# Kernel tuning notes

Measured on AMD Instinct MI355X. Metric: run time of the kernel, lower is better.

Reference implementation:

```python
import jax, jax.numpy as jnp
import numpy as np

MARGIN = 40.0


def setup_inputs() -> dict:
    key = jax.random.key(0)
    k1, k2 = jax.random.split(key)
    feat = jax.random.normal(k1, (4096, 512), dtype=jnp.float32)
    targets = jax.random.randint(k2, (4096,), 0, 64, dtype=jnp.int64)
    return {"feat": feat, "targets": targets}


def reference(feat, targets):
    # corr: (n, n) Gram matrix of features
    corr = feat @ feat.T
    # mask[i, j] = True if same class
    mask = targets[:, None] == targets[None, :]
    big = jnp.asarray(jnp.finfo(corr.dtype).max, corr.dtype)
    # per-row min over positives, max over negatives
    corr_ap = jnp.min(jnp.where(mask, corr, big), axis=1)
    corr_an = jnp.max(jnp.where(mask, -big, corr), axis=1)
    # MarginRankingLoss(margin=40) with y = 1: mean(relu(-(ap - an) + margin))
    loss = jnp.mean(jax.nn.relu(corr_an - corr_ap + MARGIN))
    return loss
```

## Files before the change

### kernel.cpp

```cpp
#include <hip/hip_runtime.h>
#include <float.h>
#include <stdint.h>


#define N_ROWS 4096
#define D_K    512
#define BM     128
#define BN     128
#define BK     32
#define NJT    (N_ROWS / BN)
#define MARGIN 40.0f

typedef __bf16 bf16_t;
typedef bf16_t bf16x8 __attribute__((ext_vector_type(8)));
typedef float  floatx4 __attribute__((ext_vector_type(4)));
typedef unsigned short ushort_t;

#define GLOAD_LDS16(g, l)                                        \
    __builtin_amdgcn_global_load_lds(                            \
        (const __attribute__((address_space(1))) void*)(g),      \
        (__attribute__((address_space(3))) void*)(l), 16, 0, 0)

__device__ __forceinline__ ushort_t f2bf_rne(float x) {
    uint32_t u = __builtin_bit_cast(uint32_t, x);
    return (ushort_t)((u + 0x7FFFu + ((u >> 16) & 1u)) >> 16);
}

typedef ushort_t ushortx8 __attribute__((ext_vector_type(8)));

__global__ __launch_bounds__(256) void cast_kernel(
    const float* __restrict__ f, ushort_t* __restrict__ o)
{
    const int i = (blockIdx.x * 256 + threadIdx.x) * 8;
    const float4 v0 = *(const float4*)(f + i);
    const float4 v1 = *(const float4*)(f + i + 4);
    ushortx8 r;
    r[0] = f2bf_rne(v0.x); r[1] = f2bf_rne(v0.y);
    r[2] = f2bf_rne(v0.z); r[3] = f2bf_rne(v0.w);
    r[4] = f2bf_rne(v1.x); r[5] = f2bf_rne(v1.y);
    r[6] = f2bf_rne(v1.z); r[7] = f2bf_rne(v1.w);
    *(ushortx8*)(o + i) = r;
}

__global__ __launch_bounds__(256) void gram_mfma_kernel(
    const ushort_t* __restrict__ fb, const int* __restrict__ tgt,
    float* __restrict__ ap_part, float* __restrict__ an_part)
{
    __shared__ __align__(16) ushort_t As[BM * BK];
    __shared__ __align__(16) ushort_t Bs[BN * BK];
    __shared__ int tgI[BM];
    __shared__ int tgJ[BN];
    __shared__ float apRed[2][BM];
    __shared__ float anRed[2][BM];

    const int tid  = threadIdx.x;
    const int i0   = blockIdx.y * BM;
    const int j0   = blockIdx.x * BN;
    const int lane = tid & 63;
    const int wave = tid >> 6;
    const int wr   = wave >> 1;
    const int wc   = wave & 1;
    const int lr   = lane & 15;
    const int lg   = lane >> 4;

    if (tid < BM)            tgI[tid]       = tgt[i0 + tid];
    else if (tid < BM + BN)  tgJ[tid - BM]  = tgt[j0 + tid - BM];

    const int srow = tid >> 2;
    const int skq  = tid & 3;
    const size_t gA0 = (size_t)(i0 + srow) * D_K + skq * 8;
    const size_t gB0 = (size_t)(j0 + srow) * D_K + skq * 8;
    char* AsB = (char*)As;
    char* BsB = (char*)Bs;

    floatx4 acc[4][4];
#pragma unroll
    for (int a = 0; a < 4; ++a)
#pragma unroll
        for (int b = 0; b < 4; ++b) acc[a][b] = (floatx4)0.0f;

    for (int k0 = 0; k0 < D_K; k0 += BK) {
        GLOAD_LDS16(fb + gA0 + k0,               AsB + tid * 16);
        GLOAD_LDS16(fb + gA0 + k0 + 64 * D_K,    AsB + 4096 + tid * 16);
        GLOAD_LDS16(fb + gB0 + k0,               BsB + tid * 16);
        GLOAD_LDS16(fb + gB0 + k0 + 64 * D_K,    BsB + 4096 + tid * 16);
        __syncthreads();

        bf16x8 af[4], bf[4];
#pragma unroll
        for (int rg = 0; rg < 4; ++rg)
            af[rg] = *(const bf16x8*)(As + ((wr * 64 + rg * 16 + lr) * BK + lg * 8));
#pragma unroll
        for (int cg = 0; cg < 4; ++cg)
            bf[cg] = *(const bf16x8*)(Bs + ((wc * 64 + cg * 16 + lr) * BK + lg * 8));
#pragma unroll
        for (int rg = 0; rg < 4; ++rg)
#pragma unroll
            for (int cg = 0; cg < 4; ++cg)
                acc[rg][cg] = __builtin_amdgcn_mfma_f32_16x16x32_bf16(
                    af[rg], bf[cg], acc[rg][cg], 0, 0, 0);
        __syncthreads();
    }

    int tj[4];
#pragma unroll
    for (int cg = 0; cg < 4; ++cg) tj[cg] = tgJ[wc * 64 + cg * 16 + lr];

#pragma unroll
    for (int rg = 0; rg < 4; ++rg) {
#pragma unroll
        for (int r = 0; r < 4; ++r) {
            const int rloc = wr * 64 + rg * 16 + lg * 4 + r;
            const int ti = tgI[rloc];
            float vap = FLT_MAX, van = -FLT_MAX;
#pragma unroll
            for (int cg = 0; cg < 4; ++cg) {
                const float v = acc[rg][cg][r];
                if (ti == tj[cg]) vap = fminf(vap, v);
                else              van = fmaxf(van, v);
            }
#pragma unroll
            for (int m = 1; m < 16; m <<= 1) {
                vap = fminf(vap, __shfl_xor(vap, m));
                van = fmaxf(van, __shfl_xor(van, m));
            }
            if (lr == 0) { apRed[wc][rloc] = vap; anRed[wc][rloc] = van; }
        }
    }
    __syncthreads();

    if (tid < BM) {
        ap_part[(size_t)blockIdx.x * N_ROWS + i0 + tid] =
            fminf(apRed[0][tid], apRed[1][tid]);
        an_part[(size_t)blockIdx.x * N_ROWS + i0 + tid] =
            fmaxf(anRed[0][tid], anRed[1][tid]);
    }
}

__global__ __launch_bounds__(256) void fold_kernel(
    const float* __restrict__ ap_part, const float* __restrict__ an_part,
    float* __restrict__ out)
{
    __shared__ float sred[4];
    const int tid = threadIdx.x;
    const int row = blockIdx.x * 256 + tid;
    float ap = FLT_MAX, an = -FLT_MAX;
#pragma unroll
    for (int js = 0; js < NJT; ++js) {
        ap = fminf(ap, ap_part[(size_t)js * N_ROWS + row]);
        an = fmaxf(an, an_part[(size_t)js * N_ROWS + row]);
    }
    const float v = an - ap + MARGIN;
    float s = (v > 0.0f) ? v : 0.0f;
#pragma unroll
    for (int m = 32; m >= 1; m >>= 1) s += __shfl_down(s, m);
    if ((tid & 63) == 0) sred[tid >> 6] = s;
    __syncthreads();
    if (tid == 0)
        atomicAdd(out, (sred[0] + sred[1] + sred[2] + sred[3]) * (1.0f / N_ROWS));
}

extern "C" void kernel_launch(void* const* d_in, const int* in_sizes, int n_in,
                              void* d_out, int out_size, void* d_ws, size_t ws_size,
                              hipStream_t stream)
{
    const float* feat = (const float*)d_in[0];
    const int*   tgt  = (const int*)d_in[1];

    ushort_t* fb      = (ushort_t*)d_ws;
    float*    ap_part = (float*)(fb + (size_t)N_ROWS * D_K);
    float*    an_part = ap_part + (size_t)NJT * N_ROWS;

    cast_kernel<<<(N_ROWS * D_K) / (256 * 8), 256, 0, stream>>>(feat, fb);

    dim3 grid(N_ROWS / BN, N_ROWS / BM);
    gram_mfma_kernel<<<grid, 256, 0, stream>>>(fb, tgt, ap_part, an_part);

    hipMemsetAsync(d_out, 0, sizeof(float), stream);
    fold_kernel<<<N_ROWS / 256, 256, 0, stream>>>(ap_part, an_part, (float*)d_out);
}
```

Baseline: 105.3 us.

## Exploit Gram matrix symmetry by computing only upper-triangular tiles

The Gram kernel now launches only the upper-triangular 128x128 tiles, about half of the original grid. Each off-diagonal tile also produces column-wise min/max reductions, which are written as partials for the transposed rows. The fold kernel becomes a single 1024-thread block that writes the result directly, removing the memset and the atomic. This roughly halves the MFMA work, at the cost of extra epilogue reductions, a small serial tile-index decode loop, and a serialized fold in one block.

```diff
diff --git a/kernel.cpp b/kernel.cpp
--- a/kernel.cpp
+++ b/kernel.cpp
@@ -8,13 +8,15 @@
 #define BM     128
 #define BN     128
 #define BK     32
-#define NJT    (N_ROWS / BN)
+#define NTB    32
+#define NTILES (NTB * (NTB + 1) / 2)
 #define MARGIN 40.0f
 
 typedef __bf16 bf16_t;
 typedef bf16_t bf16x8 __attribute__((ext_vector_type(8)));
 typedef float  floatx4 __attribute__((ext_vector_type(4)));
 typedef unsigned short ushort_t;
+typedef ushort_t ushortx8 __attribute__((ext_vector_type(8)));
 
 #define GLOAD_LDS16(g, l)                                        \
     __builtin_amdgcn_global_load_lds(                            \
@@ -25,8 +27,6 @@
     uint32_t u = __builtin_bit_cast(uint32_t, x);
     return (ushort_t)((u + 0x7FFFu + ((u >> 16) & 1u)) >> 16);
 }
-
-typedef ushort_t ushortx8 __attribute__((ext_vector_type(8)));
 
 __global__ __launch_bounds__(256) void cast_kernel(
     const float* __restrict__ f, ushort_t* __restrict__ o)
@@ -50,12 +50,16 @@
     __shared__ __align__(16) ushort_t Bs[BN * BK];
     __shared__ int tgI[BM];
     __shared__ int tgJ[BN];
-    __shared__ float apRed[2][BM];
-    __shared__ float anRed[2][BM];
+    __shared__ float apRed[2][BM],  anRed[2][BM];
+    __shared__ float apRedT[2][BN], anRedT[2][BN];
+
+    int bi = 0, rem = blockIdx.x;
+    while (rem >= NTB - bi) { rem -= NTB - bi; ++bi; }
+    const int bj = bi + rem;
 
     const int tid  = threadIdx.x;
-    const int i0   = blockIdx.y * BM;
-    const int j0   = blockIdx.x * BN;
+    const int i0   = bi * BM;
+    const int j0   = bj * BN;
     const int lane = tid & 63;
     const int wave = tid >> 6;
     const int wr   = wave >> 1;
@@ -63,8 +67,8 @@
     const int lr   = lane & 15;
     const int lg   = lane >> 4;
 
-    if (tid < BM)            tgI[tid]       = tgt[i0 + tid];
-    else if (tid < BM + BN)  tgJ[tid - BM]  = tgt[j0 + tid - BM];
+    if (tid < BM)            tgI[tid]      = tgt[i0 + tid];
+    else if (tid < BM + BN)  tgJ[tid - BM] = tgt[j0 + tid - BM];
 
     const int srow = tid >> 2;
     const int skq  = tid & 3;
@@ -80,10 +84,10 @@
         for (int b = 0; b < 4; ++b) acc[a][b] = (floatx4)0.0f;
 
     for (int k0 = 0; k0 < D_K; k0 += BK) {
-        GLOAD_LDS16(fb + gA0 + k0,               AsB + tid * 16);
-        GLOAD_LDS16(fb + gA0 + k0 + 64 * D_K,    AsB + 4096 + tid * 16);
-        GLOAD_LDS16(fb + gB0 + k0,               BsB + tid * 16);
-        GLOAD_LDS16(fb + gB0 + k0 + 64 * D_K,    BsB + 4096 + tid * 16);
+        GLOAD_LDS16(fb + gA0 + k0,            AsB + tid * 16);
+        GLOAD_LDS16(fb + gA0 + k0 + 64 * D_K, AsB + 4096 + tid * 16);
+        GLOAD_LDS16(fb + gB0 + k0,            BsB + tid * 16);
+        GLOAD_LDS16(fb + gB0 + k0 + 64 * D_K, BsB + 4096 + tid * 16);
         __syncthreads();
 
         bf16x8 af[4], bf[4];
@@ -106,6 +110,10 @@
 #pragma unroll
     for (int cg = 0; cg < 4; ++cg) tj[cg] = tgJ[wc * 64 + cg * 16 + lr];
 
+    float apT[4], anT[4];
+#pragma unroll
+    for (int cg = 0; cg < 4; ++cg) { apT[cg] = FLT_MAX; anT[cg] = -FLT_MAX; }
+
 #pragma unroll
     for (int rg = 0; rg < 4; ++rg) {
 #pragma unroll
@@ -116,8 +124,8 @@
 #pragma unroll
             for (int cg = 0; cg < 4; ++cg) {
                 const float v = acc[rg][cg][r];
-                if (ti == tj[cg]) vap = fminf(vap, v);
-                else              van = fmaxf(van, v);
+                if (ti == tj[cg]) { vap = fminf(vap, v); apT[cg] = fminf(apT[cg], v); }
+                else              { van = fmaxf(van, v); anT[cg] = fmaxf(anT[cg], v); }
             }
 #pragma unroll
             for (int m = 1; m < 16; m <<= 1) {
@@ -127,37 +135,55 @@
             if (lr == 0) { apRed[wc][rloc] = vap; anRed[wc][rloc] = van; }
         }
     }
+#pragma unroll
+    for (int cg = 0; cg < 4; ++cg) {
+        float vap = apT[cg], van = anT[cg];
+        vap = fminf(vap, __shfl_xor(vap, 16)); van = fmaxf(van, __shfl_xor(van, 16));
+        vap = fminf(vap, __shfl_xor(vap, 32)); van = fmaxf(van, __shfl_xor(van, 32));
+        if (lg == 0) {
+            apRedT[wr][wc * 64 + cg * 16 + lr] = vap;
+            anRedT[wr][wc * 64 + cg * 16 + lr] = van;
+        }
+    }
     __syncthreads();
 
     if (tid < BM) {
-        ap_part[(size_t)blockIdx.x * N_ROWS + i0 + tid] =
-            fminf(apRed[0][tid], apRed[1][tid]);
-        an_part[(size_t)blockIdx.x * N_ROWS + i0 + tid] =
-            fmaxf(anRed[0][tid], anRed[1][tid]);
-    }
-}
-
-__global__ __launch_bounds__(256) void fold_kernel(
+        ap_part[(size_t)bj * N_ROWS + i0 + tid] = fminf(apRed[0][tid], apRed[1][tid]);
+        an_part[(size_t)bj * N_ROWS + i0 + tid] = fmaxf(anRed[0][tid], anRed[1][tid]);
+        if (bi != bj) {
+            ap_part[(size_t)bi * N_ROWS + j0 + tid] = fminf(apRedT[0][tid], apRedT[1][tid]);
+            an_part[(size_t)bi * N_ROWS + j0 + tid] = fmaxf(anRedT[0][tid], anRedT[1][tid]);
+        }
+    }
+}
+
+__global__ __launch_bounds__(1024) void fold_kernel(
     const float* __restrict__ ap_part, const float* __restrict__ an_part,
     float* __restrict__ out)
 {
-    __shared__ float sred[4];
+    __shared__ float sred[16];
     const int tid = threadIdx.x;
-    const int row = blockIdx.x * 256 + tid;
-    float ap = FLT_MAX, an = -FLT_MAX;
-#pragma unroll
-    for (int js = 0; js < NJT; ++js) {
-        ap = fminf(ap, ap_part[(size_t)js * N_ROWS + row]);
-        an = fmaxf(an, an_part[(size_t)js * N_ROWS + row]);
-    }
-    const float v = an - ap + MARGIN;
-    float s = (v > 0.0f) ? v : 0.0f;
-#pragma unroll
-    for (int m = 32; m >= 1; m >>= 1) s += __shfl_down(s, m);
-    if ((tid & 63) == 0) sred[tid >> 6] = s;
+    float local = 0.0f;
+    for (int row = tid; row < N_ROWS; row += 1024) {
+        float ap = FLT_MAX, an = -FLT_MAX;
+#pragma unroll
+        for (int js = 0; js < NTB; ++js) {
+            ap = fminf(ap, ap_part[(size_t)js * N_ROWS + row]);
+            an = fmaxf(an, an_part[(size_t)js * N_ROWS + row]);
+        }
+        const float v = an - ap + MARGIN;
+        local += (v > 0.0f) ? v : 0.0f;
+    }
+#pragma unroll
+    for (int m = 32; m >= 1; m >>= 1) local += __shfl_down(local, m);
+    if ((tid & 63) == 0) sred[tid >> 6] = local;
     __syncthreads();
-    if (tid == 0)
-        atomicAdd(out, (sred[0] + sred[1] + sred[2] + sred[3]) * (1.0f / N_ROWS));
+    if (tid == 0) {
+        float s = 0.0f;
+#pragma unroll
+        for (int w = 0; w < 16; ++w) s += sred[w];
+        out[0] = s * (1.0f / N_ROWS);
+    }
 }
 
 extern "C" void kernel_launch(void* const* d_in, const int* in_sizes, int n_in,
@@ -169,13 +195,9 @@
 
     ushort_t* fb      = (ushort_t*)d_ws;
     float*    ap_part = (float*)(fb + (size_t)N_ROWS * D_K);
-    float*    an_part = ap_part + (size_t)NJT * N_ROWS;
+    float*    an_part = ap_part + (size_t)NTB * N_ROWS;
 
     cast_kernel<<<(N_ROWS * D_K) / (256 * 8), 256, 0, stream>>>(feat, fb);
-
-    dim3 grid(N_ROWS / BN, N_ROWS / BM);
-    gram_mfma_kernel<<<grid, 256, 0, stream>>>(fb, tgt, ap_part, an_part);
-
-    hipMemsetAsync(d_out, 0, sizeof(float), stream);
-    fold_kernel<<<N_ROWS / 256, 256, 0, stream>>>(ap_part, an_part, (float*)d_out);
-}
+    gram_mfma_kernel<<<NTILES, 256, 0, stream>>>(fb, tgt, ap_part, an_part);
+    fold_kernel<<<1, 1024, 0, stream>>>(ap_part, an_part, (float*)d_out);
+}
```

New measurement: 116.3 us. 1.1x slower.
